# Kernel optimization log

Measured on AMD Instinct MI355X. Metric: run time of the kernel, lower is better.

Reference implementation:

```python
import jax, jax.numpy as jnp
import numpy as np

T, D, H, E, K = 8192, 1024, 1024, 8, 2
N = T * K  # total dispatched rows


def setup_inputs() -> dict:
    key = jax.random.key(0)
    ks = jax.random.split(key, 12)
    s = 1.0 / np.sqrt(D)
    inp = {
        # uniform, contiguous per-expert segments: 2048 rows each
        'offsets': jnp.arange(E + 1, dtype=jnp.int64 if jax.config.jax_enable_x64 else jnp.int32) * (N // E),
        'jagged': jax.random.normal(ks[0], (T, D), jnp.float32),
        'weight': jax.random.normal(ks[1], (E, D, H), jnp.float32) * s,
        'bias': jax.random.normal(ks[2], (E, H), jnp.float32) * 0.02,
        'index': jax.random.randint(ks[3], (N,), 0, T),
        'weight_p': jax.random.normal(ks[4], (E, D, H), jnp.float32) * s,
        'weight_out': jax.random.normal(ks[5], (E, H, D), jnp.float32) * (1.0 / np.sqrt(H)),
        'reverse_index': jax.random.randint(ks[6], (T, K), 0, N),
        'gates': jax.random.uniform(ks[7], (N,), jnp.float32),
        'gates_index': jax.random.randint(ks[8], (T, K), 0, N),
        'bias_p': jax.random.normal(ks[9], (E, H), jnp.float32) * 0.02,
        'bias_out': jax.random.normal(ks[10], (E, D), jnp.float32) * 0.02,
    }
    return inp


def reference(offsets, jagged, weight, bias, index, weight_p, weight_out,
              reverse_index, gates, gates_index, bias_p, bias_out):
    # dispatch: gather token features into expert-sorted order  [N, D]
    x = jagged[index]
    n = x.shape[0]
    n_experts = weight.shape[0]
    # contiguous segment id per dispatched row
    expert_id = jnp.searchsorted(offsets, jnp.arange(n), side='right') - 1
    y = jnp.zeros((n, weight_out.shape[-1]), dtype=x.dtype)
    for e in range(n_experts):  # fixed small expert count
        m = (expert_id == e)[:, None].astype(x.dtype)
        xe = x * m
        g = xe @ weight[e] + bias[e]        # gate proj  [N, H]
        u = xe @ weight_p[e] + bias_p[e]    # up proj    [N, H]
        h = jax.nn.silu(g) * u              # SwiGLU
        y = y + (h @ weight_out[e] + bias_out[e]) * m
    # combine: gather K expert outputs per token, weight by gates  [T, D]
    gathered = y[reverse_index]             # [T, K, D]
    gv = gates[gates_index]                 # [T, K]
    return jnp.einsum('tkd,tk->td', gathered, gv)
```

## Files before the change

### kernel.cpp

```cpp
#include <hip/hip_runtime.h>
#include <hip/hip_bf16.h>

#define T_TOK 8192
#define DDIM 1024
#define HDIM 1024
#define NEXP 8
#define KTOP 2
#define NROWS (T_TOK * KTOP)

typedef __attribute__((ext_vector_type(8))) short bf16x8;
typedef __attribute__((ext_vector_type(4))) float f32x4;

__device__ __forceinline__ unsigned short f2bf(float f) {
    unsigned u = __builtin_bit_cast(unsigned, f);
    u += 0x7fffu + ((u >> 16) & 1u);
    return (unsigned short)(u >> 16);
}
__device__ __forceinline__ float bf2f(unsigned short h) {
    return __builtin_bit_cast(float, (unsigned)h << 16);
}

__device__ __forceinline__ void gll16(const unsigned short* g, const unsigned short* l) {
    __builtin_amdgcn_global_load_lds(
        (const __attribute__((address_space(1))) unsigned int*)g,
        (__attribute__((address_space(3))) unsigned int*)l, 16, 0, 0);
}


__global__ __launch_bounds__(256) void cvt_bf16_k(const float* __restrict__ in,
                                                  unsigned short* __restrict__ out, int n4) {
    int i = blockIdx.x * 256 + threadIdx.x;
    if (i >= n4) return;
    float4 v = ((const float4*)in)[i];
    ushort4 o;
    o.x = f2bf(v.x); o.y = f2bf(v.y); o.z = f2bf(v.z); o.w = f2bf(v.w);
    ((ushort4*)out)[i] = o;
}

__global__ __launch_bounds__(256) void transpose_cast_k(const float* __restrict__ in,
                                                        unsigned short* __restrict__ out,
                                                        int R, int C) {
    __shared__ unsigned short tile[32][33];
    int m = blockIdx.z;
    const float* src = in + (size_t)m * R * C;
    unsigned short* dst = out + (size_t)m * R * C;
    int c0 = blockIdx.x * 32, r0 = blockIdx.y * 32;
    int tx = threadIdx.x & 31, ty = threadIdx.x >> 5;
#pragma unroll
    for (int i = 0; i < 32; i += 8)
        tile[ty + i][tx] = f2bf(src[(size_t)(r0 + ty + i) * C + c0 + tx]);
    __syncthreads();
#pragma unroll
    for (int i = 0; i < 32; i += 8)
        dst[(size_t)(c0 + ty + i) * R + r0 + tx] = tile[tx][ty + i];
}


constexpr int BM2 = 256, BN2 = 256, BK2 = 32;
constexpr int NT2 = DDIM / BK2;

template <int VARIANT>
__global__ __launch_bounds__(512) void gemm256_1b_k(
    const unsigned short* __restrict__ A, const int* __restrict__ rowidx, int lda,
    const unsigned short* __restrict__ Bt, const float* __restrict__ biasE,
    const unsigned short* __restrict__ Gin, unsigned short* __restrict__ Out,
    const int* __restrict__ offsets, int N, int K) {
    __shared__ __attribute__((aligned(16))) unsigned short lds[65536];

    const int nbn = N / BN2;
    int l = (blockIdx.x & 7) * 32 + (blockIdx.x >> 3);
    int brow = l / nbn, bcol = l % nbn;
    int row0 = brow * BM2, col0 = bcol * BN2;
    int e = 0;
    while (offsets[e + 1] <= row0) ++e;

    const unsigned short* Bte = Bt + (size_t)e * N * K;
    const float* bias = biasE + (size_t)e * N;

    int tid = threadIdx.x;
    int lane = tid & 63, wid = tid >> 6;
    int wm = wid >> 2, wn = wid & 3;
    int l15 = lane & 15, l4 = lane >> 4;

    int sc = (lane & 7) ^ (lane >> 3);
    int srow = ((lane >> 3) << 1) + (sc >> 2);
    int scol = (sc & 3) * 8;
    const unsigned short* asrc[2];
    const unsigned short* bsrc[2];
#pragma unroll
    for (int q = 0; q < 2; ++q) {
        int gr = row0 + (wid * 2 + q) * 16 + srow;
        int ar = rowidx ? rowidx[gr] : gr;
        asrc[q] = A + (size_t)ar * lda + scol;
        bsrc[q] = Bte + (size_t)(col0 + (wid * 2 + q) * 16 + srow) * K + scol;
    }
    unsigned adst[2], bdst[2];
#pragma unroll
    for (int q = 0; q < 2; ++q) {
        adst[q] = (wid * 2 + q) * 512;
        bdst[q] = 32768 + (wid * 2 + q) * 512;
    }

#define STAGE(t) { int _b = (t) & 3; int _k = (t) * BK2;              \
        gll16(asrc[0] + _k, lds + _b * 8192 + adst[0]);               \
        gll16(asrc[1] + _k, lds + _b * 8192 + adst[1]);               \
        gll16(bsrc[0] + _k, lds + _b * 8192 + bdst[0]);               \
        gll16(bsrc[1] + _k, lds + _b * 8192 + bdst[1]); }

    int rdoff = (l15 >> 1) * 128 + ((((l15 & 1) << 2) | l4) ^ (l15 >> 1)) * 16;

    f32x4 acc[8][4] = {};

    STAGE(0) STAGE(1) STAGE(2)
    asm volatile("s_waitcnt vmcnt(8)" ::: "memory");
    __builtin_amdgcn_s_barrier();

#pragma unroll 1
    for (int t = 0; t < NT2; ++t) {
        const char* Ab = (const char*)lds + (t & 3) * 16384;
        const char* Bb = (const char*)lds + 65536 + (t & 3) * 16384;
        if (t + 3 < NT2) STAGE(t + 3)
        bf16x8 af[8], bfr[4];
#pragma unroll
        for (int mi = 0; mi < 8; ++mi)
            af[mi] = *(const bf16x8*)(Ab + (wm * 64 + mi * 8) * 128 + rdoff);
#pragma unroll
        for (int ni = 0; ni < 4; ++ni)
            bfr[ni] = *(const bf16x8*)(Bb + (wn * 32 + ni * 8) * 128 + rdoff);
        asm volatile("s_waitcnt lgkmcnt(0)" ::: "memory");
        __builtin_amdgcn_sched_barrier(0);
        __builtin_amdgcn_s_setprio(1);
#pragma unroll
        for (int mi = 0; mi < 8; ++mi)
#pragma unroll
            for (int ni = 0; ni < 4; ++ni)
                acc[mi][ni] = __builtin_amdgcn_mfma_f32_16x16x32_bf16(
                    af[mi], bfr[ni], acc[mi][ni], 0, 0, 0);
        __builtin_amdgcn_s_setprio(0);
        if (t < NT2 - 1) {
            if (t + 3 < NT2)       asm volatile("s_waitcnt vmcnt(8)" ::: "memory");
            else if (t + 3 == NT2) asm volatile("s_waitcnt vmcnt(4)" ::: "memory");
            else                   asm volatile("s_waitcnt vmcnt(0)" ::: "memory");
            __builtin_amdgcn_s_barrier();
        }
    }
#undef STAGE

    float bv[4];
#pragma unroll
    for (int ni = 0; ni < 4; ++ni)
        bv[ni] = bias[col0 + wn * 64 + ni * 16 + l15];

#pragma unroll
    for (int mi = 0; mi < 8; ++mi) {
        int orow_b = row0 + wm * 128 + mi * 16 + l4 * 4;
#pragma unroll
        for (int ni = 0; ni < 4; ++ni) {
            int ocol = col0 + wn * 64 + ni * 16 + l15;
#pragma unroll
            for (int q = 0; q < 4; ++q) {
                size_t oidx = (size_t)(orow_b + q) * N + ocol;
                float v = acc[mi][ni][q] + bv[ni];
                if (VARIANT == 1) {
                    float g = bf2f(Gin[oidx]);
                    float s = g / (1.0f + __expf(-g));
                    v = s * v;
                }
                Out[oidx] = f2bf(v);
            }
        }
    }
}


__global__ __launch_bounds__(256) void combine_k(
    const unsigned short* __restrict__ Y, const int* __restrict__ rev,
    const float* __restrict__ gates, const int* __restrict__ gidx,
    float* __restrict__ out) {
    int t = blockIdx.x;
    int r0 = rev[2 * t], r1 = rev[2 * t + 1];
    float g0 = gates[gidx[2 * t]], g1 = gates[gidx[2 * t + 1]];
    const unsigned short* y0 = Y + (size_t)r0 * DDIM;
    const unsigned short* y1 = Y + (size_t)r1 * DDIM;
    int d = threadIdx.x * 4;
    ushort4 a = *(const ushort4*)(y0 + d);
    ushort4 b = *(const ushort4*)(y1 + d);
    float4 r;
    r.x = g0 * bf2f(a.x) + g1 * bf2f(b.x);
    r.y = g0 * bf2f(a.y) + g1 * bf2f(b.y);
    r.z = g0 * bf2f(a.z) + g1 * bf2f(b.z);
    r.w = g0 * bf2f(a.w) + g1 * bf2f(b.w);
    *(float4*)(out + (size_t)t * DDIM + d) = r;
}


extern "C" void kernel_launch(void* const* d_in, const int* in_sizes, int n_in,
                              void* d_out, int out_size, void* d_ws, size_t ws_size,
                              hipStream_t stream) {
    const int* offsets = (const int*)d_in[0];
    const float* jagged = (const float*)d_in[1];
    const float* weight = (const float*)d_in[2];
    const float* bias = (const float*)d_in[3];
    const int* index = (const int*)d_in[4];
    const float* weight_p = (const float*)d_in[5];
    const float* weight_out = (const float*)d_in[6];
    const int* rev = (const int*)d_in[7];
    const float* gates = (const float*)d_in[8];
    const int* gidx = (const int*)d_in[9];
    const float* bias_p = (const float*)d_in[10];
    const float* bias_out = (const float*)d_in[11];
    float* out = (float*)d_out;

    char* w = (char*)d_ws;
    unsigned short* jag_bf = (unsigned short*)w; w += (size_t)T_TOK * DDIM * 2;
    unsigned short* W1t    = (unsigned short*)w; w += (size_t)NEXP * DDIM * HDIM * 2;
    unsigned short* Wpt    = (unsigned short*)w; w += (size_t)NEXP * DDIM * HDIM * 2;
    unsigned short* Wot    = (unsigned short*)w; w += (size_t)NEXP * HDIM * DDIM * 2;
    unsigned short* g_ws   = (unsigned short*)w; w += (size_t)NROWS * HDIM * 2;
    unsigned short* h_ws   = (unsigned short*)w; w += (size_t)NROWS * HDIM * 2;
    unsigned short* y_ws   = g_ws;

    cvt_bf16_k<<<(T_TOK * DDIM / 4 + 255) / 256, 256, 0, stream>>>(jagged, jag_bf, T_TOK * DDIM / 4);
    transpose_cast_k<<<dim3(HDIM / 32, DDIM / 32, NEXP), 256, 0, stream>>>(weight, W1t, DDIM, HDIM);
    transpose_cast_k<<<dim3(HDIM / 32, DDIM / 32, NEXP), 256, 0, stream>>>(weight_p, Wpt, DDIM, HDIM);
    transpose_cast_k<<<dim3(DDIM / 32, HDIM / 32, NEXP), 256, 0, stream>>>(weight_out, Wot, HDIM, DDIM);

    const int grid = (NROWS / BM2) * (HDIM / BN2);

    gemm256_1b_k<0><<<grid, 512, 0, stream>>>(jag_bf, index, DDIM, W1t, bias, nullptr, g_ws,
                                              offsets, HDIM, DDIM);
    gemm256_1b_k<1><<<grid, 512, 0, stream>>>(jag_bf, index, DDIM, Wpt, bias_p, g_ws, h_ws,
                                              offsets, HDIM, DDIM);
    gemm256_1b_k<0><<<grid, 512, 0, stream>>>(h_ws, nullptr, HDIM, Wot, bias_out, nullptr, y_ws,
                                              offsets, DDIM, HDIM);
    combine_k<<<T_TOK, 256, 0, stream>>>(y_ws, rev, gates, gidx, out);
}
```

Baseline: 180.9 us.

## Split GEMM k-step into two half-MFMA phases with double-buffered B fragments

Restructures the main GEMM loop so each k-tile runs in two halves. LDS reads for the second half of A and for the next tile's B fragments are issued while the first half's MFMAs execute. The B fragments are kept in ping-pong registers across iterations, and the global-load wait depth is tightened. This aims to hide LDS read latency behind matrix-core work, at the cost of more live registers and a tighter vmcnt wait that may stall on global loads earlier.

```diff
diff --git a/kernel.cpp b/kernel.cpp
--- a/kernel.cpp
+++ b/kernel.cpp
@@ -60,7 +60,7 @@
 constexpr int NT2 = DDIM / BK2;
 
 template <int VARIANT>
-__global__ __launch_bounds__(512) void gemm256_1b_k(
+__global__ __launch_bounds__(512) void gemm256_dp_k(
     const unsigned short* __restrict__ A, const int* __restrict__ rowidx, int lda,
     const unsigned short* __restrict__ Bt, const float* __restrict__ biasE,
     const unsigned short* __restrict__ Gin, unsigned short* __restrict__ Out,
@@ -110,40 +110,60 @@
     int rdoff = (l15 >> 1) * 128 + ((((l15 & 1) << 2) | l4) ^ (l15 >> 1)) * 16;
 
     f32x4 acc[8][4] = {};
+    bf16x8 fbA[4], fbB[4];
 
     STAGE(0) STAGE(1) STAGE(2)
-    asm volatile("s_waitcnt vmcnt(8)" ::: "memory");
+    asm volatile("s_waitcnt vmcnt(4)" ::: "memory");
     __builtin_amdgcn_s_barrier();
+#pragma unroll
+    for (int ni = 0; ni < 4; ++ni)
+        fbA[ni] = *(const bf16x8*)((const char*)lds + 65536 + (wn * 32 + ni * 8) * 128 + rdoff);
+
+#define SUBITER(T, FBC, FBN)                                              \
+    {                                                                     \
+        const char* Ab_ = (const char*)lds + ((T) & 3) * 16384;           \
+        bf16x8 fa[4], fa2[4];                                             \
+        _Pragma("unroll") for (int mi = 0; mi < 4; ++mi)                  \
+            fa[mi] = *(const bf16x8*)(Ab_ + (wm * 64 + mi * 8) * 128 + rdoff); \
+        if ((T) + 3 < NT2) STAGE((T) + 3)                                 \
+        asm volatile("s_waitcnt lgkmcnt(0)" ::: "memory");                \
+        __builtin_amdgcn_sched_barrier(0);                                \
+        __builtin_amdgcn_s_setprio(1);                                    \
+        _Pragma("unroll") for (int mi = 0; mi < 4; ++mi)                  \
+        _Pragma("unroll") for (int ni = 0; ni < 4; ++ni)                  \
+            acc[mi][ni] = __builtin_amdgcn_mfma_f32_16x16x32_bf16(        \
+                fa[mi], FBC[ni], acc[mi][ni], 0, 0, 0);                   \
+        __builtin_amdgcn_s_setprio(0);                                    \
+        _Pragma("unroll") for (int mi = 0; mi < 4; ++mi)                  \
+            fa2[mi] = *(const bf16x8*)(Ab_ + (wm * 64 + 32 + mi * 8) * 128 + rdoff); \
+        if ((T) + 1 < NT2) {                                              \
+            const char* Bb_ = (const char*)lds + 65536 + (((T) + 1) & 3) * 16384; \
+            _Pragma("unroll") for (int ni = 0; ni < 4; ++ni)              \
+                FBN[ni] = *(const bf16x8*)(Bb_ + (wn * 32 + ni * 8) * 128 + rdoff); \
+            asm volatile("s_waitcnt lgkmcnt(4)" ::: "memory");            \
+        } else {                                                          \
+            asm volatile("s_waitcnt lgkmcnt(0)" ::: "memory");            \
+        }                                                                 \
+        __builtin_amdgcn_sched_barrier(0);                                \
+        __builtin_amdgcn_s_setprio(1);                                    \
+        _Pragma("unroll") for (int mi = 0; mi < 4; ++mi)                  \
+        _Pragma("unroll") for (int ni = 0; ni < 4; ++ni)                  \
+            acc[4 + mi][ni] = __builtin_amdgcn_mfma_f32_16x16x32_bf16(    \
+                fa2[mi], FBC[ni], acc[4 + mi][ni], 0, 0, 0);              \
+        __builtin_amdgcn_s_setprio(0);                                    \
+        if ((T) + 2 < NT2) {                                              \
+            if ((T) + 3 < NT2) asm volatile("s_waitcnt vmcnt(4)" ::: "memory"); \
+            else               asm volatile("s_waitcnt vmcnt(0)" ::: "memory"); \
+            __builtin_amdgcn_s_barrier();                                 \
+        }                                                                 \
+    }
 
 #pragma unroll 1
-    for (int t = 0; t < NT2; ++t) {
-        const char* Ab = (const char*)lds + (t & 3) * 16384;
-        const char* Bb = (const char*)lds + 65536 + (t & 3) * 16384;
-        if (t + 3 < NT2) STAGE(t + 3)
-        bf16x8 af[8], bfr[4];
-#pragma unroll
-        for (int mi = 0; mi < 8; ++mi)
-            af[mi] = *(const bf16x8*)(Ab + (wm * 64 + mi * 8) * 128 + rdoff);
-#pragma unroll
-        for (int ni = 0; ni < 4; ++ni)
-            bfr[ni] = *(const bf16x8*)(Bb + (wn * 32 + ni * 8) * 128 + rdoff);
-        asm volatile("s_waitcnt lgkmcnt(0)" ::: "memory");
-        __builtin_amdgcn_sched_barrier(0);
-        __builtin_amdgcn_s_setprio(1);
-#pragma unroll
-        for (int mi = 0; mi < 8; ++mi)
-#pragma unroll
-            for (int ni = 0; ni < 4; ++ni)
-                acc[mi][ni] = __builtin_amdgcn_mfma_f32_16x16x32_bf16(
-                    af[mi], bfr[ni], acc[mi][ni], 0, 0, 0);
-        __builtin_amdgcn_s_setprio(0);
-        if (t < NT2 - 1) {
-            if (t + 3 < NT2)       asm volatile("s_waitcnt vmcnt(8)" ::: "memory");
-            else if (t + 3 == NT2) asm volatile("s_waitcnt vmcnt(4)" ::: "memory");
-            else                   asm volatile("s_waitcnt vmcnt(0)" ::: "memory");
-            __builtin_amdgcn_s_barrier();
-        }
-    }
+    for (int i = 0; i < NT2 / 2; ++i) {
+        SUBITER(2 * i,     fbA, fbB)
+        SUBITER(2 * i + 1, fbB, fbA)
+    }
+#undef SUBITER
 #undef STAGE
 
     float bv[4];
@@ -227,11 +247,11 @@
 
     const int grid = (NROWS / BM2) * (HDIM / BN2);
 
-    gemm256_1b_k<0><<<grid, 512, 0, stream>>>(jag_bf, index, DDIM, W1t, bias, nullptr, g_ws,
+    gemm256_dp_k<0><<<grid, 512, 0, stream>>>(jag_bf, index, DDIM, W1t, bias, nullptr, g_ws,
                                               offsets, HDIM, DDIM);
-    gemm256_1b_k<1><<<grid, 512, 0, stream>>>(jag_bf, index, DDIM, Wpt, bias_p, g_ws, h_ws,
+    gemm256_dp_k<1><<<grid, 512, 0, stream>>>(jag_bf, index, DDIM, Wpt, bias_p, g_ws, h_ws,
                                               offsets, HDIM, DDIM);
-    gemm256_1b_k<0><<<grid, 512, 0, stream>>>(h_ws, nullptr, HDIM, Wot, bias_out, nullptr, y_ws,
+    gemm256_dp_k<0><<<grid, 512, 0, stream>>>(h_ws, nullptr, HDIM, Wot, bias_out, nullptr, y_ws,
                                               offsets, DDIM, HDIM);
     combine_k<<<T_TOK, 256, 0, stream>>>(y_ws, rev, gates, gidx, out);
 }
```

Measured after the change: 180.1 us. About the same (-0.4%).
